# Optimization experiments

Hardware: AMD Instinct MI355X
Metric: run time of the kernel (lower is better)

## Reference

```python
import jax, jax.numpy as jnp
import numpy as np

def setup_inputs() -> dict:
    key = jax.random.key(0)
    k1, k2, k3 = jax.random.split(key, 3)
    N, C, H, W = 16, 128, 128, 128
    out_chn = 128
    x = jax.random.normal(k1, (N, C, H, W), dtype=jnp.float32)
    # 1x1 conv = per-pixel linear: weight (out_chn, in_chn), bias (out_chn,)
    fan_in = C  # kernel_size=1 -> fan_in = in_chn
    bound = 1.0 / np.sqrt(fan_in)
    conv_w = jax.random.uniform(k2, (out_chn, C), dtype=jnp.float32, minval=-bound, maxval=bound)
    conv_b = jax.random.uniform(k3, (out_chn,), dtype=jnp.float32, minval=-bound, maxval=bound)
    return {"x": x, "conv_w": conv_w, "conv_b": conv_b}

def reference(x, conv_w, conv_b):
    N, C, H, W = x.shape
    x_hw = x.reshape(N, C, H * W)                     # (N, C, HW)
    logits = jnp.einsum('ncl,ndl->ncd', x_hw, x_hw)    # (N, C, C), unscaled
    weights = jax.nn.softmax(logits, axis=-1)
    attn = jnp.einsum('ncd,ndl->ncl', weights, x_hw)   # (N, C, HW)
    attn = attn.reshape(N, C, H, W)
    # 1x1 conv: contract over channel dim
    out = jnp.einsum('nchw,oc->nohw', attn, conv_w) + conv_b[None, :, None, None]
    return out
```

## Files before the change

### kernel.cpp

```cpp
#include <hip/hip_runtime.h>
#include <hip/hip_bf16.h>
#include <stdint.h>

#define NB    16
#define CD    128
#define HW    16384
#define KSPLIT 32

typedef float  f32x4  __attribute__((ext_vector_type(4)));
typedef short  bf16x8 __attribute__((ext_vector_type(8)));

__device__ __forceinline__ unsigned f2bf(float f) {
    unsigned u = __float_as_uint(f);
    u += 0x7FFFu + ((u >> 16) & 1u);
    return u >> 16;
}

__global__ __launch_bounds__(256) void gram_kernel(const float* __restrict__ x,
                                                   float* __restrict__ P) {
    const int n  = blockIdx.x;
    const int kc = blockIdx.y;
    const int t    = threadIdx.x;
    const int wv   = t >> 6;
    const int lane = t & 63;
    const int q    = lane >> 4;
    const int r16  = lane & 15;

    __shared__ __align__(16) unsigned short Xl[CD * 132];

    f32x4 acc[4][4];
#pragma unroll
    for (int i = 0; i < 4; ++i)
#pragma unroll
        for (int j = 0; j < 4; ++j) acc[i][j] = (f32x4)0.0f;

    const int rt0 = 4 * (wv >> 1);
    const int ct0 = 4 * (wv & 1);

    const float* xb = x + (size_t)n * CD * HW;

    for (int sub = 0; sub < 4; ++sub) {
        const int kbase = kc * 512 + sub * 128;
#pragma unroll
        for (int i = 0; i < 16; ++i) {
            int f  = i * 256 + t;
            int c  = f >> 5;
            int l4 = (f & 31) * 4;
            float4 v = *(const float4*)(xb + (size_t)c * HW + kbase + l4);
            uint2 pk;
            pk.x = f2bf(v.x) | (f2bf(v.y) << 16);
            pk.y = f2bf(v.z) | (f2bf(v.w) << 16);
            *(uint2*)(&Xl[c * 132 + l4]) = pk;
        }
        __syncthreads();

#pragma unroll
        for (int ks = 0; ks < 4; ++ks) {
            const int k0 = ks * 32 + q * 8;
            bf16x8 af[4], bfr[4];
#pragma unroll
            for (int i = 0; i < 4; ++i) {
                const unsigned short* pa = &Xl[(16 * (rt0 + i) + r16) * 132 + k0];
                union { bf16x8 v; uint2 u[2]; } ua;
                ua.u[0] = *(const uint2*)pa;
                ua.u[1] = *(const uint2*)(pa + 4);
                af[i] = ua.v;
                const unsigned short* pb = &Xl[(16 * (ct0 + i) + r16) * 132 + k0];
                union { bf16x8 v; uint2 u[2]; } ub;
                ub.u[0] = *(const uint2*)pb;
                ub.u[1] = *(const uint2*)(pb + 4);
                bfr[i] = ub.v;
            }
#pragma unroll
            for (int i = 0; i < 4; ++i)
#pragma unroll
                for (int j = 0; j < 4; ++j)
                    acc[i][j] = __builtin_amdgcn_mfma_f32_16x16x32_bf16(
                        af[i], bfr[j], acc[i][j], 0, 0, 0);
        }
        __syncthreads();
    }

    float* Pn = P + ((size_t)kc * NB + n) * CD * CD;
#pragma unroll
    for (int i = 0; i < 4; ++i)
#pragma unroll
        for (int j = 0; j < 4; ++j)
#pragma unroll
            for (int rr = 0; rr < 4; ++rr) {
                int row = 16 * (rt0 + i) + q * 4 + rr;
                int col = 16 * (ct0 + j) + r16;
                Pn[row * CD + col] = acc[i][j][rr];
            }
}

__global__ __launch_bounds__(256) void reduce_kernel(const float* __restrict__ P,
                                                     float* __restrict__ G,
                                                     float* __restrict__ mx,
                                                     float* __restrict__ rs) {
    const int R    = blockIdx.x * 4 + (threadIdx.x >> 6);
    const int lane = threadIdx.x & 63;
    const int n    = R >> 7;
    const int row  = R & 127;

    const float* p = P + (size_t)n * CD * CD + (size_t)row * CD;
    float s0 = 0.0f, s1 = 0.0f;
#pragma unroll
    for (int kc = 0; kc < KSPLIT; ++kc) {
        const float* pk = p + (size_t)kc * NB * CD * CD;
        s0 += pk[lane];
        s1 += pk[lane + 64];
    }
    float m = fmaxf(s0, s1);
#pragma unroll
    for (int off = 32; off > 0; off >>= 1) m = fmaxf(m, __shfl_xor(m, off));
    float e = __expf(s0 - m) + __expf(s1 - m);
#pragma unroll
    for (int off = 32; off > 0; off >>= 1) e += __shfl_xor(e, off);

    float* g = G + (size_t)n * CD * CD + (size_t)row * CD;
    g[lane]      = s0;
    g[lane + 64] = s1;
    if (lane == 0) {
        mx[R] = m;
        rs[R] = 1.0f / e;
    }
}

__global__ __launch_bounds__(256) void mmat_kernel(const float* __restrict__ G,
                                                   const float* __restrict__ mx,
                                                   const float* __restrict__ rs,
                                                   const float* __restrict__ cw,
                                                   unsigned short* __restrict__ Mbf) {
    const int n  = blockIdx.x;
    const int bo = blockIdx.y;
    const int t  = threadIdx.x;
    __shared__ __align__(16) float Wl[CD * CD];

    const float* Gn  = G  + (size_t)n * CD * CD;
    const float* mxn = mx + n * CD;
    const float* rsn = rs + n * CD;

#pragma unroll 4
    for (int i = 0; i < 64; ++i) {
        int e = i * 256 + t;
        int c = e >> 7;
        int d = e & 127;
        Wl[c * CD + d] = __expf(Gn[c * CD + d] - mxn[c]) * rsn[c];
    }
    __syncthreads();

    const int o  = bo * 16 + (t >> 4);
    const int d0 = (t & 15) * 8;
    float a0 = 0, a1 = 0, a2 = 0, a3 = 0, a4 = 0, a5 = 0, a6 = 0, a7 = 0;
    const float* cwo = cw + (size_t)o * CD;
#pragma unroll 4
    for (int c = 0; c < CD; ++c) {
        float cv = cwo[c];
        float4 w0 = *(const float4*)&Wl[c * CD + d0];
        float4 w1 = *(const float4*)&Wl[c * CD + d0 + 4];
        a0 += cv * w0.x; a1 += cv * w0.y; a2 += cv * w0.z; a3 += cv * w0.w;
        a4 += cv * w1.x; a5 += cv * w1.y; a6 += cv * w1.z; a7 += cv * w1.w;
    }
    uint4 pk;
    pk.x = f2bf(a0) | (f2bf(a1) << 16);
    pk.y = f2bf(a2) | (f2bf(a3) << 16);
    pk.z = f2bf(a4) | (f2bf(a5) << 16);
    pk.w = f2bf(a6) | (f2bf(a7) << 16);
    *(uint4*)&Mbf[((size_t)n * CD + o) * CD + d0] = pk;
}

__global__ __launch_bounds__(256) void out_kernel(const float* __restrict__ x,
                                                  const unsigned short* __restrict__ Mbf,
                                                  const float* __restrict__ bias,
                                                  float* __restrict__ out) {
    const int lb = blockIdx.x;
    const int n  = blockIdx.y;
    const int l0 = lb * 128;
    const int t    = threadIdx.x;
    const int wv   = t >> 6;
    const int lane = t & 63;
    const int q    = lane >> 4;
    const int r16  = lane & 15;

    __shared__ __align__(16) unsigned short Xt[128 * 128];
    __shared__ float bl[CD];

    const int lt0 = 4 * (wv >> 1);
    const int ot0 = 4 * (wv & 1);

    if (t < CD) bl[t] = bias[t];

    const float* xb = x + (size_t)n * CD * HW + l0;
    const int lt = t & 31;
    const int dg = t >> 5;
#pragma unroll
    for (int i = 0; i < 4; ++i) {
        const int d0 = i * 32 + dg * 4;
        const float* bp = xb + (size_t)d0 * HW + 4 * lt;
        float4 v0 = *(const float4*)(bp);
        float4 v1 = *(const float4*)(bp + HW);
        float4 v2 = *(const float4*)(bp + 2 * HW);
        float4 v3 = *(const float4*)(bp + 3 * HW);
        float r0[4] = {v0.x, v0.y, v0.z, v0.w};
        float r1[4] = {v1.x, v1.y, v1.z, v1.w};
        float r2[4] = {v2.x, v2.y, v2.z, v2.w};
        float r3[4] = {v3.x, v3.y, v3.z, v3.w};
        const int dph = d0 ^ (8 * (lt & 7));
#pragma unroll
        for (int j = 0; j < 4; ++j) {
            uint2 pk;
            pk.x = f2bf(r0[j]) | (f2bf(r1[j]) << 16);
            pk.y = f2bf(r2[j]) | (f2bf(r3[j]) << 16);
            *(uint2*)&Xt[(4 * lt + j) * 128 + dph] = pk;
        }
    }
    __syncthreads();

    f32x4 acc[4][4];
#pragma unroll
    for (int i = 0; i < 4; ++i)
#pragma unroll
        for (int j = 0; j < 4; ++j) acc[i][j] = (f32x4)0.0f;

    const unsigned short* Mn = Mbf + (size_t)n * CD * CD;
#pragma unroll
    for (int ks = 0; ks < 4; ++ks) {
        const int k0 = ks * 32 + q * 8;
        bf16x8 bfr[4];
#pragma unroll
        for (int j = 0; j < 4; ++j) {
            const int o = 16 * (ot0 + j) + r16;
            union { bf16x8 v; uint4 u; } ub;
            ub.u = *(const uint4*)&Mn[o * CD + k0];
            bfr[j] = ub.v;
        }
        bf16x8 af[4];
#pragma unroll
        for (int i = 0; i < 4; ++i) {
            const int l = 16 * (lt0 + i) + r16;
            const int doff = k0 ^ (8 * ((l >> 2) & 7));
            union { bf16x8 v; uint4 u; } ua;
            ua.u = *(const uint4*)&Xt[l * 128 + doff];
            af[i] = ua.v;
        }
#pragma unroll
        for (int i = 0; i < 4; ++i)
#pragma unroll
            for (int j = 0; j < 4; ++j)
                acc[i][j] = __builtin_amdgcn_mfma_f32_16x16x32_bf16(
                    af[i], bfr[j], acc[i][j], 0, 0, 0);
    }

    float* ob = out + (size_t)n * CD * HW + l0;
#pragma unroll
    for (int i = 0; i < 4; ++i)
#pragma unroll
        for (int j = 0; j < 4; ++j) {
            const int o = 16 * (ot0 + j) + r16;
            const int l = 16 * (lt0 + i) + q * 4;
            const float b = bl[o];
            float4 st;
            st.x = acc[i][j][0] + b;
            st.y = acc[i][j][1] + b;
            st.z = acc[i][j][2] + b;
            st.w = acc[i][j][3] + b;
            *(float4*)(ob + (size_t)o * HW + l) = st;
        }
}

extern "C" void kernel_launch(void* const* d_in, const int* in_sizes, int n_in,
                              void* d_out, int out_size, void* d_ws, size_t ws_size,
                              hipStream_t stream) {
    const float* x  = (const float*)d_in[0];
    const float* cw = (const float*)d_in[1];
    const float* cb = (const float*)d_in[2];
    float* out = (float*)d_out;

    char* ws = (char*)d_ws;
    float*          P   = (float*)(ws);
    float*          G   = (float*)(ws + (32u << 20));
    float*          mxp = (float*)(ws + (33u << 20));
    float*          rsp = (float*)(ws + (33u << 20) + 8192);
    unsigned short* Mbf = (unsigned short*)(ws + (33u << 20) + 16384);

    gram_kernel   <<<dim3(NB, KSPLIT), 256, 0, stream>>>(x, P);
    reduce_kernel <<<dim3(512),        256, 0, stream>>>(P, G, mxp, rsp);
    mmat_kernel   <<<dim3(NB, 8),      256, 0, stream>>>(G, mxp, rsp, cw, Mbf);
    out_kernel    <<<dim3(128, NB),    256, 0, stream>>>(x, Mbf, cb, out);
}
```

Baseline: 306.8 us.

## Prefetch gram tiles into registers; move softmax normalization into reduce kernel

The gram kernel now loads the next 128-column slab of x into registers while the MFMA loop runs on the current LDS tile, aiming to hide global-load latency, and it sets a launch-bounds occupancy hint of 2. The softmax exponent and normalization move into the reduce kernel, which writes normalized weights directly. The mmat kernel therefore skips its per-block exp recompute and LDS staging, reading E from global memory with twice as many blocks. The register staging raises register pressure in the gram kernel.

```diff
diff --git a/kernel.cpp b/kernel.cpp
--- a/kernel.cpp
+++ b/kernel.cpp
@@ -16,8 +16,12 @@
     return u >> 16;
 }
 
-__global__ __launch_bounds__(256) void gram_kernel(const float* __restrict__ x,
-                                                   float* __restrict__ P) {
+__device__ __forceinline__ unsigned pk2bf(float a, float b) {
+    return f2bf(a) | (f2bf(b) << 16);
+}
+
+__global__ __launch_bounds__(256, 2) void gram_kernel(const float* __restrict__ x,
+                                                      float* __restrict__ P) {
     const int n  = blockIdx.x;
     const int kc = blockIdx.y;
     const int t    = threadIdx.x;
@@ -39,20 +43,30 @@
 
     const float* xb = x + (size_t)n * CD * HW;
 
+    const int cS = t >> 5;
+    const int lS = (t & 31) * 4;
+
+    float4 stg[16];
+#pragma unroll
+    for (int i = 0; i < 16; ++i)
+        stg[i] = *(const float4*)(xb + (size_t)(i * 8 + cS) * HW + kc * 512 + lS);
+
     for (int sub = 0; sub < 4; ++sub) {
-        const int kbase = kc * 512 + sub * 128;
 #pragma unroll
         for (int i = 0; i < 16; ++i) {
-            int f  = i * 256 + t;
-            int c  = f >> 5;
-            int l4 = (f & 31) * 4;
-            float4 v = *(const float4*)(xb + (size_t)c * HW + kbase + l4);
             uint2 pk;
-            pk.x = f2bf(v.x) | (f2bf(v.y) << 16);
-            pk.y = f2bf(v.z) | (f2bf(v.w) << 16);
-            *(uint2*)(&Xl[c * 132 + l4]) = pk;
+            pk.x = pk2bf(stg[i].x, stg[i].y);
+            pk.y = pk2bf(stg[i].z, stg[i].w);
+            *(uint2*)(&Xl[(i * 8 + cS) * 132 + lS]) = pk;
         }
         __syncthreads();
+
+        if (sub < 3) {
+            const int kb = kc * 512 + (sub + 1) * 128;
+#pragma unroll
+            for (int i = 0; i < 16; ++i)
+                stg[i] = *(const float4*)(xb + (size_t)(i * 8 + cS) * HW + kb + lS);
+        }
 
 #pragma unroll
         for (int ks = 0; ks < 4; ++ks) {
@@ -95,9 +109,7 @@
 }
 
 __global__ __launch_bounds__(256) void reduce_kernel(const float* __restrict__ P,
-                                                     float* __restrict__ G,
-                                                     float* __restrict__ mx,
-                                                     float* __restrict__ rs) {
+                                                     float* __restrict__ E) {
     const int R    = blockIdx.x * 4 + (threadIdx.x >> 6);
     const int lane = threadIdx.x & 63;
     const int n    = R >> 7;
@@ -114,60 +126,41 @@
     float m = fmaxf(s0, s1);
 #pragma unroll
     for (int off = 32; off > 0; off >>= 1) m = fmaxf(m, __shfl_xor(m, off));
-    float e = __expf(s0 - m) + __expf(s1 - m);
+    const float e0 = __expf(s0 - m);
+    const float e1 = __expf(s1 - m);
+    float e = e0 + e1;
 #pragma unroll
     for (int off = 32; off > 0; off >>= 1) e += __shfl_xor(e, off);
-
-    float* g = G + (size_t)n * CD * CD + (size_t)row * CD;
-    g[lane]      = s0;
-    g[lane + 64] = s1;
-    if (lane == 0) {
-        mx[R] = m;
-        rs[R] = 1.0f / e;
-    }
-}
-
-__global__ __launch_bounds__(256) void mmat_kernel(const float* __restrict__ G,
-                                                   const float* __restrict__ mx,
-                                                   const float* __restrict__ rs,
+    const float inv = 1.0f / e;
+
+    float* g = E + (size_t)n * CD * CD + (size_t)row * CD;
+    g[lane]      = e0 * inv;
+    g[lane + 64] = e1 * inv;
+}
+
+__global__ __launch_bounds__(256) void mmat_kernel(const float* __restrict__ E,
                                                    const float* __restrict__ cw,
                                                    unsigned short* __restrict__ Mbf) {
     const int n  = blockIdx.x;
     const int bo = blockIdx.y;
     const int t  = threadIdx.x;
-    __shared__ __align__(16) float Wl[CD * CD];
-
-    const float* Gn  = G  + (size_t)n * CD * CD;
-    const float* mxn = mx + n * CD;
-    const float* rsn = rs + n * CD;
-
-#pragma unroll 4
-    for (int i = 0; i < 64; ++i) {
-        int e = i * 256 + t;
-        int c = e >> 7;
-        int d = e & 127;
-        Wl[c * CD + d] = __expf(Gn[c * CD + d] - mxn[c]) * rsn[c];
-    }
-    __syncthreads();
-
-    const int o  = bo * 16 + (t >> 4);
-    const int d0 = (t & 15) * 8;
-    float a0 = 0, a1 = 0, a2 = 0, a3 = 0, a4 = 0, a5 = 0, a6 = 0, a7 = 0;
+    const int o  = bo * 8 + (t >> 5);
+    const int d0 = (t & 31) * 4;
+
+    const float* En  = E + (size_t)n * CD * CD;
     const float* cwo = cw + (size_t)o * CD;
-#pragma unroll 4
+
+    float a0 = 0, a1 = 0, a2 = 0, a3 = 0;
+#pragma unroll 8
     for (int c = 0; c < CD; ++c) {
-        float cv = cwo[c];
-        float4 w0 = *(const float4*)&Wl[c * CD + d0];
-        float4 w1 = *(const float4*)&Wl[c * CD + d0 + 4];
-        a0 += cv * w0.x; a1 += cv * w0.y; a2 += cv * w0.z; a3 += cv * w0.w;
-        a4 += cv * w1.x; a5 += cv * w1.y; a6 += cv * w1.z; a7 += cv * w1.w;
-    }
-    uint4 pk;
-    pk.x = f2bf(a0) | (f2bf(a1) << 16);
-    pk.y = f2bf(a2) | (f2bf(a3) << 16);
-    pk.z = f2bf(a4) | (f2bf(a5) << 16);
-    pk.w = f2bf(a6) | (f2bf(a7) << 16);
-    *(uint4*)&Mbf[((size_t)n * CD + o) * CD + d0] = pk;
+        const float cv = cwo[c];
+        float4 w = *(const float4*)&En[c * CD + d0];
+        a0 += cv * w.x; a1 += cv * w.y; a2 += cv * w.z; a3 += cv * w.w;
+    }
+    uint2 pk;
+    pk.x = pk2bf(a0, a1);
+    pk.y = pk2bf(a2, a3);
+    *(uint2*)&Mbf[((size_t)n * CD + o) * CD + d0] = pk;
 }
 
 __global__ __launch_bounds__(256) void out_kernel(const float* __restrict__ x,
@@ -210,8 +203,8 @@
 #pragma unroll
         for (int j = 0; j < 4; ++j) {
             uint2 pk;
-            pk.x = f2bf(r0[j]) | (f2bf(r1[j]) << 16);
-            pk.y = f2bf(r2[j]) | (f2bf(r3[j]) << 16);
+            pk.x = pk2bf(r0[j], r1[j]);
+            pk.y = pk2bf(r2[j], r3[j]);
             *(uint2*)&Xt[(4 * lt + j) * 128 + dph] = pk;
         }
     }
@@ -279,13 +272,11 @@
 
     char* ws = (char*)d_ws;
     float*          P   = (float*)(ws);
-    float*          G   = (float*)(ws + (32u << 20));
-    float*          mxp = (float*)(ws + (33u << 20));
-    float*          rsp = (float*)(ws + (33u << 20) + 8192);
-    unsigned short* Mbf = (unsigned short*)(ws + (33u << 20) + 16384);
+    float*          E   = (float*)(ws + (32u << 20));
+    unsigned short* Mbf = (unsigned short*)(ws + (33u << 20));
 
     gram_kernel   <<<dim3(NB, KSPLIT), 256, 0, stream>>>(x, P);
-    reduce_kernel <<<dim3(512),        256, 0, stream>>>(P, G, mxp, rsp);
-    mmat_kernel   <<<dim3(NB, 8),      256, 0, stream>>>(G, mxp, rsp, cw, Mbf);
+    reduce_kernel <<<dim3(512),        256, 0, stream>>>(P, E);
+    mmat_kernel   <<<dim3(NB, 16),     256, 0, stream>>>(E, cw, Mbf);
     out_kernel    <<<dim3(128, NB),    256, 0, stream>>>(x, Mbf, cb, out);
 }
```

Result: no change. 303.4 us (-1.1%).
